# Kernel tuning notes

Hardware: AMD Instinct MI355X
Metric: run time of the kernel (lower is better)

The kernel has to match this reference:

```python
import jax, jax.numpy as jnp
import numpy as np
from functools import partial

MATCH_THRESHOLD = 0.3
EPS = 1e-12  # torch F.normalize eps


def _embed(x, W1, b1, W2, b2):
    h = jax.nn.relu(x @ W1 + b1)
    e = h @ W2 + b2
    n = jnp.maximum(jnp.linalg.norm(e, axis=-1, keepdims=True), EPS)
    return e / n


def setup_inputs() -> dict:
    key = jax.random.key(0)
    ks = jax.random.split(key, 4)
    N_t, N_t1, D, E = 8192, 8192, 4, 64
    return {
        "detections_t": jax.random.normal(ks[0], (N_t, D), jnp.float32),
        "detections_t1": jax.random.normal(ks[1], (N_t1, D), jnp.float32),
        "W1": jax.random.normal(ks[2], (D, E), jnp.float32) / np.sqrt(D),
        "b1": jnp.zeros((E,), jnp.float32),
        "W2": jax.random.normal(ks[3], (E, E), jnp.float32) / np.sqrt(E),
        "b2": jnp.zeros((E,), jnp.float32),
    }


def reference(detections_t, detections_t1, W1, b1, W2, b2):
    e_t = _embed(detections_t, W1, b1, W2, b2)    # (N_t, E)
    e_t1 = _embed(detections_t1, W1, b1, W2, b2)  # (N_t1, E)
    sim = e_t @ e_t1.T                            # (N_t, N_t1)

    N_t, N_t1 = sim.shape
    max_sims = jnp.max(sim, axis=1)
    max_idxs = jnp.argmax(sim, axis=1)
    order = jnp.argsort(-max_sims)  # descending by best similarity

    matches0 = jnp.full((N_t,), -1, dtype=jnp.int32)
    used0 = jnp.zeros((N_t1,), dtype=jnp.bool_)

    def step(carry, i):
        matches, used = carry
        j = max_idxs[i]
        ok = jnp.logical_and(~used[j], max_sims[i] > MATCH_THRESHOLD)
        matches = matches.at[i].set(jnp.where(ok, j.astype(jnp.int32), matches[i]))
        used = used.at[j].set(used[j] | ok)
        return (matches, used), None

    (matches, _), _ = jax.lax.scan(step, (matches0, used0), order)
    return matches, sim
```

## Files before the change

### kernel.cpp

```cpp
#include <hip/hip_runtime.h>
#include <stdint.h>

#define N_DET 8192
#define E_DIM 64
#define LSTR 132

__device__ __forceinline__ unsigned fmap(float x) {
    unsigned b = __float_as_uint(x);
    return (b & 0x80000000u) ? ~b : (b | 0x80000000u);
}
__device__ __forceinline__ unsigned long long umax64(unsigned long long a, unsigned long long b) {
    return a > b ? a : b;
}

__global__ __launch_bounds__(256) void k_embed(
    const float* __restrict__ dt, const float* __restrict__ dt1,
    const float* __restrict__ W1, const float* __restrict__ b1,
    const float* __restrict__ W2, const float* __restrict__ b2,
    float* __restrict__ eout)
{
    int wave = (blockIdx.x * 256 + threadIdx.x) >> 6;
    int lane = threadIdx.x & 63;
    if (wave >= 2 * N_DET) return;
    const float* src = (wave < N_DET) ? (dt + (size_t)wave * 4)
                                      : (dt1 + (size_t)(wave - N_DET) * 4);
    float x0 = src[0], x1 = src[1], x2 = src[2], x3 = src[3];
    float h = b1[lane];
    h = fmaf(x0, W1[lane],        h);
    h = fmaf(x1, W1[64  + lane],  h);
    h = fmaf(x2, W1[128 + lane],  h);
    h = fmaf(x3, W1[192 + lane],  h);
    h = fmaxf(h, 0.0f);
    float e = b2[lane];
    #pragma unroll
    for (int k = 0; k < 64; ++k) {
        float hk = __shfl(h, k, 64);
        e = fmaf(hk, W2[k * 64 + lane], e);
    }
    float s = e * e;
    #pragma unroll
    for (int m = 32; m >= 1; m >>= 1) s += __shfl_xor(s, m, 64);
    float n = sqrtf(s);
    n = fmaxf(n, 1e-12f);
    eout[(size_t)wave * 64 + lane] = e / n;
}

__global__ __launch_bounds__(256, 2) void k_sim_fused(
    const float* __restrict__ et, const float* __restrict__ et1,
    float* __restrict__ sim, unsigned long long* __restrict__ rowkey)
{
    __shared__ float As[64 * LSTR];
    __shared__ float Bs[64 * LSTR];
    const int tid = threadIdx.x;
    const int bx = blockIdx.x, by = blockIdx.y;

    {
        const float4* ag = (const float4*)(et  + (size_t)by * 128 * 64);
        const float4* bg = (const float4*)(et1 + (size_t)bx * 128 * 64);
        #pragma unroll
        for (int i = 0; i < 8; ++i) {
            int f = tid + i * 256;
            int m = f >> 4;
            int k = (f & 15) * 4;
            float4 va = ag[f];
            As[(k + 0) * LSTR + m] = va.x;
            As[(k + 1) * LSTR + m] = va.y;
            As[(k + 2) * LSTR + m] = va.z;
            As[(k + 3) * LSTR + m] = va.w;
            float4 vb = bg[f];
            Bs[(k + 0) * LSTR + m] = vb.x;
            Bs[(k + 1) * LSTR + m] = vb.y;
            Bs[(k + 2) * LSTR + m] = vb.z;
            Bs[(k + 3) * LSTR + m] = vb.w;
        }
    }
    __syncthreads();

    const int tx = tid & 15;
    const int ty = tid >> 4;
    float acc[8][8];
    #pragma unroll
    for (int i = 0; i < 8; ++i)
        #pragma unroll
        for (int j = 0; j < 8; ++j) acc[i][j] = 0.0f;

    const float4* As4 = (const float4*)As;
    const float4* Bs4 = (const float4*)Bs;

    #pragma unroll 2
    for (int k = 0; k < 64; ++k) {
        const int base = k * 33;
        float4 a0 = As4[base + ty];
        float4 a1 = As4[base + 16 + ty];
        float4 b0 = Bs4[base + tx];
        float4 b1 = Bs4[base + 16 + tx];
        float a[8] = {a0.x, a0.y, a0.z, a0.w, a1.x, a1.y, a1.z, a1.w};
        float b[8] = {b0.x, b0.y, b0.z, b0.w, b1.x, b1.y, b1.z, b1.w};
        #pragma unroll
        for (int i = 0; i < 8; ++i)
            #pragma unroll
            for (int j = 0; j < 8; ++j)
                acc[i][j] = fmaf(a[i], b[j], acc[i][j]);
    }

    const int cbase = bx * 128;
    #pragma unroll
    for (int i = 0; i < 8; ++i) {
        int mrow = (i < 4) ? (ty * 4 + i) : (64 + ty * 4 + (i - 4));
        size_t rg = (size_t)by * 128 + mrow;
        float4* sp = (float4*)(sim + rg * N_DET + cbase);
        sp[tx]      = make_float4(acc[i][0], acc[i][1], acc[i][2], acc[i][3]);
        sp[16 + tx] = make_float4(acc[i][4], acc[i][5], acc[i][6], acc[i][7]);

        unsigned long long key = 0ull;
        #pragma unroll
        for (int j = 0; j < 8; ++j) {
            int col = cbase + ((j < 4) ? (tx * 4 + j) : (64 + tx * 4 + (j - 4)));
            unsigned long long kk =
                ((unsigned long long)fmap(acc[i][j]) << 32) | (unsigned)(~col);
            key = umax64(key, kk);
        }
        #pragma unroll
        for (int m = 1; m < 16; m <<= 1)
            key = umax64(key, __shfl_xor(key, m, 64));
        if (tx == 0) atomicMax(&rowkey[rg], key);
    }
}

__global__ void k_init(unsigned long long* __restrict__ p) {
    p[blockIdx.x * 256 + threadIdx.x] = 0ull;
}

__global__ void k_claim(const unsigned long long* __restrict__ rowkey,
                        unsigned long long* __restrict__ winner, unsigned uthr) {
    int i = blockIdx.x * 256 + threadIdx.x;
    if (i >= N_DET) return;
    unsigned long long k = rowkey[i];
    unsigned u = (unsigned)(k >> 32);
    if (u > uthr) {
        unsigned col = ~(unsigned)k;
        unsigned long long claim = ((unsigned long long)u << 32) | (~(unsigned)i);
        atomicMax(&winner[col], claim);
    }
}

__global__ void k_match(const unsigned long long* __restrict__ rowkey,
                        const unsigned long long* __restrict__ winner,
                        float* __restrict__ out, unsigned uthr) {
    int i = blockIdx.x * 256 + threadIdx.x;
    if (i >= N_DET) return;
    unsigned long long k = rowkey[i];
    unsigned u = (unsigned)(k >> 32);
    float m = -1.0f;
    if (u > uthr) {
        unsigned col = ~(unsigned)k;
        unsigned long long claim = ((unsigned long long)u << 32) | (~(unsigned)i);
        if (winner[col] == claim) m = (float)col;
    }
    out[i] = m;
}

extern "C" void kernel_launch(void* const* d_in, const int* in_sizes, int n_in,
                              void* d_out, int out_size, void* d_ws, size_t ws_size,
                              hipStream_t stream) {
    const float* dt  = (const float*)d_in[0];
    const float* dt1 = (const float*)d_in[1];
    const float* W1  = (const float*)d_in[2];
    const float* b1  = (const float*)d_in[3];
    const float* W2  = (const float*)d_in[4];
    const float* b2  = (const float*)d_in[5];

    float* out = (float*)d_out;
    float* sim = out + N_DET;

    char* ws = (char*)d_ws;
    float* et  = (float*)ws;
    float* et1 = et + (size_t)N_DET * E_DIM;
    unsigned long long* rowkey = (unsigned long long*)(ws + 2ull * N_DET * E_DIM * 4);
    unsigned long long* winner = rowkey + N_DET;

    unsigned uthr;
    { union { float f; unsigned u; } c; c.f = 0.3f; uthr = c.u | 0x80000000u; }

    k_embed<<<(2 * N_DET) / 4, 256, 0, stream>>>(dt, dt1, W1, b1, W2, b2, et);
    k_init<<<(2 * N_DET) / 256, 256, 0, stream>>>(rowkey);

    dim3 g2(N_DET / 128, N_DET / 128);
    k_sim_fused<<<g2, 256, 0, stream>>>(et, et1, sim, rowkey);

    k_claim<<<N_DET / 256, 256, 0, stream>>>(rowkey, winner, uthr);
    k_match<<<N_DET / 256, 256, 0, stream>>>(rowkey, winner, out, uthr);
}
```

Baseline: 157.9 us.

## Widen sim tiles to 128x256, reuse A tile, use nontemporal stores and per-thread argmax

Each block now covers 256 columns, processed as two 128-column halves. The A tile stays in shared memory while the B tile is reloaded between halves. Results are written with nontemporal stores, since the 256MB sim output should not pollute cache. Row-max keys are reduced within each thread with a float compare before packing, and the cross-lane shuffle and atomicMax run once per row instead of once per 128-column tile, halving global atomics. The B reload is not overlapped with compute, and the grid is halved, which lowers parallelism.

```diff
diff --git a/kernel.cpp b/kernel.cpp
--- a/kernel.cpp
+++ b/kernel.cpp
@@ -4,6 +4,8 @@
 #define N_DET 8192
 #define E_DIM 64
 #define LSTR 132
+
+typedef float f4v __attribute__((ext_vector_type(4)));
 
 __device__ __forceinline__ unsigned fmap(float x) {
     unsigned b = __float_as_uint(x);
@@ -52,78 +54,125 @@
     __shared__ float As[64 * LSTR];
     __shared__ float Bs[64 * LSTR];
     const int tid = threadIdx.x;
-    const int bx = blockIdx.x, by = blockIdx.y;
+    const int bx = blockIdx.x;
+    const int by = blockIdx.y;
+    const int tx = tid & 15;
+    const int ty = tid >> 4;
 
     {
-        const float4* ag = (const float4*)(et  + (size_t)by * 128 * 64);
-        const float4* bg = (const float4*)(et1 + (size_t)bx * 128 * 64);
+        const float4* ag = (const float4*)(et + (size_t)by * 128 * 64);
         #pragma unroll
         for (int i = 0; i < 8; ++i) {
             int f = tid + i * 256;
             int m = f >> 4;
             int k = (f & 15) * 4;
-            float4 va = ag[f];
-            As[(k + 0) * LSTR + m] = va.x;
-            As[(k + 1) * LSTR + m] = va.y;
-            As[(k + 2) * LSTR + m] = va.z;
-            As[(k + 3) * LSTR + m] = va.w;
-            float4 vb = bg[f];
-            Bs[(k + 0) * LSTR + m] = vb.x;
-            Bs[(k + 1) * LSTR + m] = vb.y;
-            Bs[(k + 2) * LSTR + m] = vb.z;
-            Bs[(k + 3) * LSTR + m] = vb.w;
+            float4 v = ag[f];
+            As[(k + 0) * LSTR + m] = v.x;
+            As[(k + 1) * LSTR + m] = v.y;
+            As[(k + 2) * LSTR + m] = v.z;
+            As[(k + 3) * LSTR + m] = v.w;
+        }
+    }
+    {
+        const float4* bg = (const float4*)(et1 + (size_t)bx * 256 * 64);
+        #pragma unroll
+        for (int i = 0; i < 8; ++i) {
+            int f = tid + i * 256;
+            int m = f >> 4;
+            int k = (f & 15) * 4;
+            float4 v = bg[f];
+            Bs[(k + 0) * LSTR + m] = v.x;
+            Bs[(k + 1) * LSTR + m] = v.y;
+            Bs[(k + 2) * LSTR + m] = v.z;
+            Bs[(k + 3) * LSTR + m] = v.w;
         }
     }
     __syncthreads();
 
-    const int tx = tid & 15;
-    const int ty = tid >> 4;
-    float acc[8][8];
-    #pragma unroll
-    for (int i = 0; i < 8; ++i)
-        #pragma unroll
-        for (int j = 0; j < 8; ++j) acc[i][j] = 0.0f;
-
-    const float4* As4 = (const float4*)As;
-    const float4* Bs4 = (const float4*)Bs;
+    unsigned long long keys[8];
+    #pragma unroll
+    for (int i = 0; i < 8; ++i) keys[i] = 0ull;
+
+    const f4v* As4 = (const f4v*)As;
+    const f4v* Bs4 = (const f4v*)Bs;
 
     #pragma unroll 2
-    for (int k = 0; k < 64; ++k) {
-        const int base = k * 33;
-        float4 a0 = As4[base + ty];
-        float4 a1 = As4[base + 16 + ty];
-        float4 b0 = Bs4[base + tx];
-        float4 b1 = Bs4[base + 16 + tx];
-        float a[8] = {a0.x, a0.y, a0.z, a0.w, a1.x, a1.y, a1.z, a1.w};
-        float b[8] = {b0.x, b0.y, b0.z, b0.w, b1.x, b1.y, b1.z, b1.w};
+    for (int t = 0; t < 2; ++t) {
+        float acc[8][8];
         #pragma unroll
         for (int i = 0; i < 8; ++i)
             #pragma unroll
-            for (int j = 0; j < 8; ++j)
-                acc[i][j] = fmaf(a[i], b[j], acc[i][j]);
-    }
-
-    const int cbase = bx * 128;
+            for (int j = 0; j < 8; ++j) acc[i][j] = 0.0f;
+
+        #pragma unroll 8
+        for (int k = 0; k < 64; ++k) {
+            const int base = k * 33;
+            f4v a0 = As4[base + ty];
+            f4v a1 = As4[base + 16 + ty];
+            f4v b0 = Bs4[base + tx];
+            f4v b1 = Bs4[base + 16 + tx];
+            float a[8] = {a0.x, a0.y, a0.z, a0.w, a1.x, a1.y, a1.z, a1.w};
+            float b[8] = {b0.x, b0.y, b0.z, b0.w, b1.x, b1.y, b1.z, b1.w};
+            #pragma unroll
+            for (int i = 0; i < 8; ++i)
+                #pragma unroll
+                for (int j = 0; j < 8; ++j)
+                    acc[i][j] = fmaf(a[i], b[j], acc[i][j]);
+        }
+
+        if (t == 0) {
+            __syncthreads();
+            const float4* bg = (const float4*)(et1 + ((size_t)bx * 256 + 128) * 64);
+            #pragma unroll
+            for (int i = 0; i < 8; ++i) {
+                int f = tid + i * 256;
+                int m = f >> 4;
+                int k = (f & 15) * 4;
+                float4 v = bg[f];
+                Bs[(k + 0) * LSTR + m] = v.x;
+                Bs[(k + 1) * LSTR + m] = v.y;
+                Bs[(k + 2) * LSTR + m] = v.z;
+                Bs[(k + 3) * LSTR + m] = v.w;
+            }
+        }
+
+        const int cbase = bx * 256 + t * 128;
+        #pragma unroll
+        for (int i = 0; i < 8; ++i) {
+            int mrow = (i < 4) ? (ty * 4 + i) : (64 + ty * 4 + (i - 4));
+            size_t rg = (size_t)by * 128 + mrow;
+            f4v* sp = (f4v*)(sim + rg * N_DET + cbase);
+            f4v v0 = {acc[i][0], acc[i][1], acc[i][2], acc[i][3]};
+            f4v v1 = {acc[i][4], acc[i][5], acc[i][6], acc[i][7]};
+            __builtin_nontemporal_store(v0, sp + tx);
+            __builtin_nontemporal_store(v1, sp + 16 + tx);
+
+            float bv = acc[i][0]; int bj = 0;
+            #pragma unroll
+            for (int j = 1; j < 8; ++j) {
+                bool c = acc[i][j] > bv;
+                bv = c ? acc[i][j] : bv;
+                bj = c ? j : bj;
+            }
+            int col = cbase + ((bj < 4) ? (tx * 4 + bj) : (64 + tx * 4 + (bj - 4)));
+            unsigned long long key =
+                ((unsigned long long)fmap(bv) << 32) | (unsigned)(~col);
+            keys[i] = umax64(keys[i], key);
+        }
+
+        if (t == 0) __syncthreads();
+    }
+
     #pragma unroll
     for (int i = 0; i < 8; ++i) {
-        int mrow = (i < 4) ? (ty * 4 + i) : (64 + ty * 4 + (i - 4));
-        size_t rg = (size_t)by * 128 + mrow;
-        float4* sp = (float4*)(sim + rg * N_DET + cbase);
-        sp[tx]      = make_float4(acc[i][0], acc[i][1], acc[i][2], acc[i][3]);
-        sp[16 + tx] = make_float4(acc[i][4], acc[i][5], acc[i][6], acc[i][7]);
-
-        unsigned long long key = 0ull;
-        #pragma unroll
-        for (int j = 0; j < 8; ++j) {
-            int col = cbase + ((j < 4) ? (tx * 4 + j) : (64 + tx * 4 + (j - 4)));
-            unsigned long long kk =
-                ((unsigned long long)fmap(acc[i][j]) << 32) | (unsigned)(~col);
-            key = umax64(key, kk);
-        }
+        unsigned long long key = keys[i];
         #pragma unroll
         for (int m = 1; m < 16; m <<= 1)
             key = umax64(key, __shfl_xor(key, m, 64));
-        if (tx == 0) atomicMax(&rowkey[rg], key);
+        if (tx == 0) {
+            int mrow = (i < 4) ? (ty * 4 + i) : (64 + ty * 4 + (i - 4));
+            atomicMax(&rowkey[(size_t)by * 128 + mrow], key);
+        }
     }
 }
 
@@ -185,7 +234,7 @@
     k_embed<<<(2 * N_DET) / 4, 256, 0, stream>>>(dt, dt1, W1, b1, W2, b2, et);
     k_init<<<(2 * N_DET) / 256, 256, 0, stream>>>(rowkey);
 
-    dim3 g2(N_DET / 128, N_DET / 128);
+    dim3 g2(N_DET / 256, N_DET / 128);
     k_sim_fused<<<g2, 256, 0, stream>>>(et, et1, sim, rowkey);
 
     k_claim<<<N_DET / 256, 256, 0, stream>>>(rowkey, winner, uthr);
```

After: 161.9 us. +2.5%, slower.

## Compute similarity with split-bf16 MFMA and rescue argmax via fp32 top-2 recheck

Applied to the files above, without the earlier changes.

Replaces the fp32 FMA tiled GEMM with v_mfma_f32_32x32x16_bf16 over three hi/lo bf16 products, which approximates fp32 precision while using the matrix cores. The per-row argmax no longer uses global atomics. Each wave keeps the top-2 candidates per 64-column chunk in LDS, and a new rescue kernel recomputes those candidates in exact fp32 to choose the row key. Operands are loaded directly from global memory with no LDS staging, and sim is written with nontemporal stores. The risk is small numeric differences in sim, plus top-2 misses if near-ties fall outside a chunk's top 2.

```diff
diff --git a/kernel.cpp b/kernel.cpp
--- a/kernel.cpp
+++ b/kernel.cpp
@@ -3,7 +3,10 @@
 
 #define N_DET 8192
 #define E_DIM 64
-#define LSTR 132
+
+typedef float  f32x16  __attribute__((ext_vector_type(16)));
+typedef short  short8v __attribute__((ext_vector_type(8)));
+typedef unsigned short ushort_t;
 
 __device__ __forceinline__ unsigned fmap(float x) {
     unsigned b = __float_as_uint(x);
@@ -11,13 +14,18 @@
 }
 __device__ __forceinline__ unsigned long long umax64(unsigned long long a, unsigned long long b) {
     return a > b ? a : b;
+}
+__device__ __forceinline__ ushort_t f2bf(float x) {
+    unsigned u = __float_as_uint(x);
+    unsigned r = u + 0x7fffu + ((u >> 16) & 1u);
+    return (ushort_t)(r >> 16);
 }
 
 __global__ __launch_bounds__(256) void k_embed(
     const float* __restrict__ dt, const float* __restrict__ dt1,
     const float* __restrict__ W1, const float* __restrict__ b1,
     const float* __restrict__ W2, const float* __restrict__ b2,
-    float* __restrict__ eout)
+    float* __restrict__ ef, ushort_t* __restrict__ ehi, ushort_t* __restrict__ elo)
 {
     int wave = (blockIdx.x * 256 + threadIdx.x) >> 6;
     int lane = threadIdx.x & 63;
@@ -42,89 +50,145 @@
     for (int m = 32; m >= 1; m >>= 1) s += __shfl_xor(s, m, 64);
     float n = sqrtf(s);
     n = fmaxf(n, 1e-12f);
-    eout[(size_t)wave * 64 + lane] = e / n;
-}
-
-__global__ __launch_bounds__(256, 2) void k_sim_fused(
-    const float* __restrict__ et, const float* __restrict__ et1,
-    float* __restrict__ sim, unsigned long long* __restrict__ rowkey)
+    float v = e / n;
+    size_t idx = (size_t)wave * 64 + lane;
+    ef[idx] = v;
+    ushort_t h16 = f2bf(v);
+    float hf = __uint_as_float(((unsigned)h16) << 16);
+    ehi[idx] = h16;
+    elo[idx] = f2bf(v - hf);
+}
+
+__global__ __launch_bounds__(256) void k_sim_mfma(
+    const ushort_t* __restrict__ ehi, const ushort_t* __restrict__ elo,
+    float* __restrict__ sim, unsigned* __restrict__ candbuf)
 {
-    __shared__ float As[64 * LSTR];
-    __shared__ float Bs[64 * LSTR];
-    const int tid = threadIdx.x;
+    __shared__ float sm[4][64][65];
+    const int tid  = threadIdx.x;
+    const int l    = tid & 63;
+    const int w    = tid >> 6;
+    const int l31  = l & 31;
+    const int half = l >> 5;
     const int bx = blockIdx.x, by = blockIdx.y;
+    const int rowbase = by * 128 + (w >> 1) * 64;
+    const int colbase = bx * 128 + (w & 1) * 64;
+
+    const size_t aoff0 = (size_t)(rowbase + l31) * 64 + half * 8;
+    const size_t aoff1 = aoff0 + (size_t)32 * 64;
+    const size_t boff0 = (size_t)(N_DET + colbase + l31) * 64 + half * 8;
+    const size_t boff1 = boff0 + (size_t)32 * 64;
+
+    f32x16 acc00 = {}; f32x16 acc01 = {}; f32x16 acc10 = {}; f32x16 acc11 = {};
+    asm volatile("s_nop 1" : "+v"(acc00), "+v"(acc01), "+v"(acc10), "+v"(acc11));
+
+    #pragma unroll
+    for (int p = 0; p < 3; ++p) {
+        const ushort_t* Ab = (p == 2) ? elo : ehi;
+        const ushort_t* Bb = (p == 1) ? elo : ehi;
+        #pragma unroll
+        for (int s = 0; s < 4; ++s) {
+            const int ko = s * 16;
+            short8v a0 = *(const short8v*)(Ab + aoff0 + ko);
+            short8v a1 = *(const short8v*)(Ab + aoff1 + ko);
+            short8v b0 = *(const short8v*)(Bb + boff0 + ko);
+            short8v b1 = *(const short8v*)(Bb + boff1 + ko);
+            asm volatile("v_mfma_f32_32x32x16_bf16 %0, %1, %2, %0"
+                         : "+v"(acc00) : "v"(a0), "v"(b0));
+            asm volatile("v_mfma_f32_32x32x16_bf16 %0, %1, %2, %0"
+                         : "+v"(acc01) : "v"(a0), "v"(b1));
+            asm volatile("v_mfma_f32_32x32x16_bf16 %0, %1, %2, %0"
+                         : "+v"(acc10) : "v"(a1), "v"(b0));
+            asm volatile("v_mfma_f32_32x32x16_bf16 %0, %1, %2, %0"
+                         : "+v"(acc11) : "v"(a1), "v"(b1));
+        }
+    }
+    asm volatile("s_nop 7\n\ts_nop 7\n\ts_nop 7"
+                 : "+v"(acc00), "+v"(acc01), "+v"(acc10), "+v"(acc11));
+
+    #pragma unroll
+    for (int reg = 0; reg < 16; ++reg) {
+        const int rowloc = (reg & 3) + ((reg >> 2) << 3) + (half << 2);
+        {
+            const int row = rowbase + rowloc;
+            float v0 = acc00[reg], v1 = acc01[reg];
+            float* sp = sim + (size_t)row * N_DET + colbase + l31;
+            __builtin_nontemporal_store(v0, sp);
+            __builtin_nontemporal_store(v1, sp + 32);
+            sm[w][rowloc][l31]      = v0;
+            sm[w][rowloc][l31 + 32] = v1;
+        }
+        {
+            const int row = rowbase + 32 + rowloc;
+            float v0 = acc10[reg], v1 = acc11[reg];
+            float* sp = sim + (size_t)row * N_DET + colbase + l31;
+            __builtin_nontemporal_store(v0, sp);
+            __builtin_nontemporal_store(v1, sp + 32);
+            sm[w][32 + rowloc][l31]      = v0;
+            sm[w][32 + rowloc][l31 + 32] = v1;
+        }
+    }
 
     {
-        const float4* ag = (const float4*)(et  + (size_t)by * 128 * 64);
-        const float4* bg = (const float4*)(et1 + (size_t)bx * 128 * 64);
+        const float* rowp = &sm[w][l][0];
+        float m1 = rowp[0], m2 = -3.0e38f;
+        int c1 = 0, c2 = 0;
         #pragma unroll
-        for (int i = 0; i < 8; ++i) {
-            int f = tid + i * 256;
-            int m = f >> 4;
-            int k = (f & 15) * 4;
-            float4 va = ag[f];
-            As[(k + 0) * LSTR + m] = va.x;
-            As[(k + 1) * LSTR + m] = va.y;
-            As[(k + 2) * LSTR + m] = va.z;
-            As[(k + 3) * LSTR + m] = va.w;
-            float4 vb = bg[f];
-            Bs[(k + 0) * LSTR + m] = vb.x;
-            Bs[(k + 1) * LSTR + m] = vb.y;
-            Bs[(k + 2) * LSTR + m] = vb.z;
-            Bs[(k + 3) * LSTR + m] = vb.w;
-        }
-    }
-    __syncthreads();
-
-    const int tx = tid & 15;
-    const int ty = tid >> 4;
-    float acc[8][8];
-    #pragma unroll
-    for (int i = 0; i < 8; ++i)
+        for (int c = 1; c < 64; ++c) {
+            float v = rowp[c];
+            bool gt1 = v > m1;
+            bool gt2 = v > m2;
+            m2 = gt1 ? m1 : (gt2 ? v : m2);
+            c2 = gt1 ? c1 : (gt2 ? c : c2);
+            m1 = gt1 ? v : m1;
+            c1 = gt1 ? c : c1;
+        }
+        const int row = rowbase + l;
+        const int cb  = bx * 2 + (w & 1);
+        unsigned cc1 = (unsigned)(colbase + c1);
+        unsigned cc2 = (unsigned)(colbase + c2);
+        candbuf[(size_t)row * 128 + cb] = (cc1 << 16) | cc2;
+    }
+}
+
+__global__ __launch_bounds__(256) void k_rescue(
+    const float* __restrict__ ef, const unsigned* __restrict__ candbuf,
+    unsigned long long* __restrict__ rowkey)
+{
+    const int row = blockIdx.x * 4 + (threadIdx.x >> 6);
+    const int l   = threadIdx.x & 63;
+    const float* et1f = ef + (size_t)N_DET * 64;
+
+    unsigned cw0 = candbuf[(size_t)row * 128 + l];
+    unsigned cw1 = candbuf[(size_t)row * 128 + 64 + l];
+    int cols[4] = { (int)(cw0 >> 16), (int)(cw0 & 0xffffu),
+                    (int)(cw1 >> 16), (int)(cw1 & 0xffffu) };
+
+    float4 q[16];
+    const float4* qp = (const float4*)(ef + (size_t)row * 64);
+    #pragma unroll
+    for (int i = 0; i < 16; ++i) q[i] = qp[i];
+
+    unsigned long long best = 0ull;
+    #pragma unroll
+    for (int c = 0; c < 4; ++c) {
+        const float4* rp = (const float4*)(et1f + (size_t)cols[c] * 64);
+        float d = 0.0f;
         #pragma unroll
-        for (int j = 0; j < 8; ++j) acc[i][j] = 0.0f;
-
-    const float4* As4 = (const float4*)As;
-    const float4* Bs4 = (const float4*)Bs;
-
-    #pragma unroll 2
-    for (int k = 0; k < 64; ++k) {
-        const int base = k * 33;
-        float4 a0 = As4[base + ty];
-        float4 a1 = As4[base + 16 + ty];
-        float4 b0 = Bs4[base + tx];
-        float4 b1 = Bs4[base + 16 + tx];
-        float a[8] = {a0.x, a0.y, a0.z, a0.w, a1.x, a1.y, a1.z, a1.w};
-        float b[8] = {b0.x, b0.y, b0.z, b0.w, b1.x, b1.y, b1.z, b1.w};
-        #pragma unroll
-        for (int i = 0; i < 8; ++i)
-            #pragma unroll
-            for (int j = 0; j < 8; ++j)
-                acc[i][j] = fmaf(a[i], b[j], acc[i][j]);
-    }
-
-    const int cbase = bx * 128;
-    #pragma unroll
-    for (int i = 0; i < 8; ++i) {
-        int mrow = (i < 4) ? (ty * 4 + i) : (64 + ty * 4 + (i - 4));
-        size_t rg = (size_t)by * 128 + mrow;
-        float4* sp = (float4*)(sim + rg * N_DET + cbase);
-        sp[tx]      = make_float4(acc[i][0], acc[i][1], acc[i][2], acc[i][3]);
-        sp[16 + tx] = make_float4(acc[i][4], acc[i][5], acc[i][6], acc[i][7]);
-
-        unsigned long long key = 0ull;
-        #pragma unroll
-        for (int j = 0; j < 8; ++j) {
-            int col = cbase + ((j < 4) ? (tx * 4 + j) : (64 + tx * 4 + (j - 4)));
-            unsigned long long kk =
-                ((unsigned long long)fmap(acc[i][j]) << 32) | (unsigned)(~col);
-            key = umax64(key, kk);
-        }
-        #pragma unroll
-        for (int m = 1; m < 16; m <<= 1)
-            key = umax64(key, __shfl_xor(key, m, 64));
-        if (tx == 0) atomicMax(&rowkey[rg], key);
-    }
+        for (int i = 0; i < 16; ++i) {
+            float4 v = rp[i];
+            d = fmaf(q[i].x, v.x, d);
+            d = fmaf(q[i].y, v.y, d);
+            d = fmaf(q[i].z, v.z, d);
+            d = fmaf(q[i].w, v.w, d);
+        }
+        unsigned long long k =
+            ((unsigned long long)fmap(d) << 32) | (unsigned)(~cols[c]);
+        best = umax64(best, k);
+    }
+    #pragma unroll
+    for (int m = 1; m < 64; m <<= 1)
+        best = umax64(best, __shfl_xor(best, m, 64));
+    if (l == 0) rowkey[row] = best;
 }
 
 __global__ void k_init(unsigned long long* __restrict__ p) {
@@ -174,20 +238,23 @@
     float* sim = out + N_DET;
 
     char* ws = (char*)d_ws;
-    float* et  = (float*)ws;
-    float* et1 = et + (size_t)N_DET * E_DIM;
-    unsigned long long* rowkey = (unsigned long long*)(ws + 2ull * N_DET * E_DIM * 4);
+    float*    ef      = (float*)ws;
+    ushort_t* ehi     = (ushort_t*)(ws + (4u << 20));
+    ushort_t* elo     = (ushort_t*)(ws + (6u << 20));
+    unsigned* candbuf = (unsigned*)(ws + (8u << 20));
+    unsigned long long* rowkey = (unsigned long long*)(ws + (12u << 20));
     unsigned long long* winner = rowkey + N_DET;
 
     unsigned uthr;
     { union { float f; unsigned u; } c; c.f = 0.3f; uthr = c.u | 0x80000000u; }
 
-    k_embed<<<(2 * N_DET) / 4, 256, 0, stream>>>(dt, dt1, W1, b1, W2, b2, et);
-    k_init<<<(2 * N_DET) / 256, 256, 0, stream>>>(rowkey);
+    k_embed<<<(2 * N_DET) / 4, 256, 0, stream>>>(dt, dt1, W1, b1, W2, b2, ef, ehi, elo);
+    k_init<<<N_DET / 256, 256, 0, stream>>>(winner);
 
     dim3 g2(N_DET / 128, N_DET / 128);
-    k_sim_fused<<<g2, 256, 0, stream>>>(et, et1, sim, rowkey);
-
+    k_sim_mfma<<<g2, 256, 0, stream>>>(ehi, elo, sim, candbuf);
+
+    k_rescue<<<N_DET / 4, 256, 0, stream>>>(ef, candbuf, rowkey);
     k_claim<<<N_DET / 256, 256, 0, stream>>>(rowkey, winner, uthr);
     k_match<<<N_DET / 256, 256, 0, stream>>>(rowkey, winner, out, uthr);
 }
```

Result: slower. 231.0 us (+46.3%).
